# Performance work log

Measured on AMD Instinct MI355X. Metric: run time of the kernel, lower is better.

## Reference

```python
import jax, jax.numpy as jnp
import numpy as np

EPS = 1e-7  # keras.backend.epsilon()
ROUTING_ITERS = 3

def squash(v, axis=-1):
    s2 = jnp.sum(jnp.square(v), axis=axis, keepdims=True)
    scale = s2 / (1.0 + s2) / jnp.sqrt(s2 + EPS)
    return scale * v

def setup_inputs() -> dict:
    key = jax.random.key(0)
    k1, k2 = jax.random.split(key)
    B, N_IN, D_IN = 128, 648, 16
    N_OUT, D_OUT = 32, 32
    x = jax.random.normal(k1, (B, N_IN, D_IN), dtype=jnp.float32)
    # glorot-uniform-ish scale for W: shape (N_in, num_caps, cap_dim, d_in)
    limit = np.sqrt(6.0 / (D_IN + D_OUT)).astype(np.float32)
    W = jax.random.uniform(k2, (N_IN, N_OUT, D_OUT, D_IN), dtype=jnp.float32,
                           minval=-limit, maxval=limit)
    return {"x": x, "W": W}

def reference(x, W):
    # prediction vectors u_hat: [B, N_in, N_out, D_out]
    # (original tiles inputs then matmuls W @ u; einsum fuses this)
    u_hat = jnp.einsum('njdi,bni->bnjd', W, x)
    B, N_in, N_out, _ = u_hat.shape
    logits = jnp.zeros((B, N_in, N_out, 1), dtype=u_hat.dtype)
    v = None
    for i in range(ROUTING_ITERS):
        c = jax.nn.softmax(logits, axis=2)                      # [B,N_in,N_out,1]
        s = jnp.sum(c * u_hat, axis=1, keepdims=True)           # [B,1,N_out,D_out]
        v = squash(s, axis=-1)                                  # [B,1,N_out,D_out]
        if i < ROUTING_ITERS - 1:
            agreement = jnp.sum(u_hat * v, axis=-1, keepdims=True)
            logits = logits + agreement
    return jnp.squeeze(v, axis=1)                               # [B,N_out,D_out]
```

## Files before the change

### kernel.cpp

```cpp
#include <hip/hip_runtime.h>
#include <hip/hip_fp16.h>
#include <math.h>


#define N_IN 648
#define ELEMS 131072

#define WF16_OFF 1048576
#define PARTS_OFF 22282240

#define PX_OFF 131072
#define LG 139264
#define ARENA 147456

typedef __attribute__((ext_vector_type(8))) _Float16 f16x8;
typedef __attribute__((ext_vector_type(16))) float f32x16;

union F16U { uint4 u; f16x8 f; };
union HU { __half h; unsigned short us; };

__device__ __forceinline__ unsigned pkh(float a, float b) {
  HU x, y; x.h = __float2half(a); y.h = __float2half(b);
  return (unsigned)x.us | ((unsigned)y.us << 16);
}
__device__ __forceinline__ float h2f(unsigned short u) {
  HU x; x.us = u; return __half2float(x.h);
}

__device__ __forceinline__ void writeW(char* wbuf, int jS, int d, const float4* r) {
  uint4 h0, h1;
  h0.x = pkh(r[0].x, r[0].y); h0.y = pkh(r[0].z, r[0].w);
  h0.z = pkh(r[1].x, r[1].y); h0.w = pkh(r[1].z, r[1].w);
  h1.x = pkh(r[2].x, r[2].y); h1.y = pkh(r[2].z, r[2].w);
  h1.z = pkh(r[3].x, r[3].y); h1.w = pkh(r[3].z, r[3].w);
  *(uint4*)(wbuf + jS * 1024 + d * 16) = h0;
  *(uint4*)(wbuf + jS * 1024 + 512 + d * 16) = h1;
}
__device__ __forceinline__ void loadW(float4* r, const float* __restrict__ W,
                                      int n, int jS, int d) {
  const float4* rp = (const float4*)(W + (size_t)n * 16384 + jS * 512 + d * 16);
  r[0] = rp[0]; r[1] = rp[1]; r[2] = rp[2]; r[3] = rp[3];
}

__global__ __launch_bounds__(512) void cvt_w_f16(const float* __restrict__ W,
                                                 char* __restrict__ wf) {
  const int n = blockIdx.x;
  const int t = threadIdx.x;
  const int jS = t >> 4, m = t & 15;
  float4 rA[4], rB[4];
  loadW(rA, W, n, jS, m);
  loadW(rB, W, n, jS, m + 16);
  char* dst = wf + (size_t)n * 32768;
  writeW(dst, jS, m, rA);
  writeW(dst, jS, m + 16, rB);
}

__device__ __forceinline__ void stage_pair(char* nwf, char* nxb,
                                           const char* __restrict__ wf16,
                                           const float* __restrict__ x,
                                           int nbase, int cnt, int b0, int t) {
  const char* src = wf16 + (size_t)nbase * 32768;
  for (int r = 0; r < cnt * 4; ++r)
    *(uint4*)(nwf + r * 8192 + t * 16) = *(const uint4*)(src + r * 8192 + t * 16);
  if (t < 128) {
    const int s2 = t >> 6, u = t & 63;
    if (s2 < cnt) {
      const float4* xp = (const float4*)(
          x + ((size_t)(b0 + (u & 31)) * N_IN + nbase + s2) * 16 + (u >> 5) * 8);
      *(float4*)(nxb + s2 * 2048 + u * 16) = xp[0];
      *(float4*)(nxb + s2 * 2048 + 1024 + u * 16) = xp[1];
    }
  }
}

__device__ __forceinline__ void store_parts(char* arena, __half* __restrict__ parts,
                                            const f32x16* acc, float scale,
                                            int nchunk, int b0, int t) {
  const int w = t >> 6, l = t & 63;
  const int b32 = l & 31, half = l >> 5;
  __syncthreads();
#pragma unroll
  for (int q = 0; q < 4; ++q) {
    const int j = w * 4 + q;
#pragma unroll
    for (int g = 0; g < 4; ++g) {
      float4 v4;
      v4.x = acc[q][g * 4 + 0] * scale;
      v4.y = acc[q][g * 4 + 1] * scale;
      v4.z = acc[q][g * 4 + 2] * scale;
      v4.w = acc[q][g * 4 + 3] * scale;
      *(float4*)(arena + (b32 * 1036 + j * 32 + g * 8 + 4 * half) * 4) = v4;
    }
  }
  __syncthreads();
  char* pb = (char*)(parts + (size_t)nchunk * ELEMS + (size_t)b0 * 1024);
  const int rb = t >> 4, c16 = t & 15;
#pragma unroll
  for (int q = 0; q < 8; ++q) {
    const int g8 = c16 + q * 16;
    const float4 a = *(const float4*)(arena + (rb * 1036 + g8 * 8) * 4);
    const float4 b = *(const float4*)(arena + (rb * 1036 + g8 * 8 + 4) * 4);
    *(uint4*)(pb + rb * 2048 + g8 * 16) =
        uint4{pkh(a.x, a.y), pkh(a.z, a.w), pkh(b.x, b.y), pkh(b.z, b.w)};
  }
}

__device__ __forceinline__ void decode_bid(int bid, int NC, int& nchunk, int& btile) {
  if ((NC & 7) == 0) {
    const int r = bid & 7;
    btile = (bid >> 3) & 3;
    nchunk = (bid >> 5) * 8 + r;
  } else {
    nchunk = bid >> 2;
    btile = bid & 3;
  }
}

__global__ __launch_bounds__(512, 1) void caps_pass0_mfma(
    const float* __restrict__ x, const char* __restrict__ wf16,
    __half* __restrict__ parts, int NC)
{
  __shared__ __align__(16) char arena[ARENA];
  const int t = threadIdx.x;
  const int w = t >> 6, l = t & 63;
  int nchunk, btile;
  decode_bid(blockIdx.x, NC, nchunk, btile);
  const int n0 = (N_IN * nchunk) / NC;
  const int n1 = (N_IN * (nchunk + 1)) / NC;
  const int b0 = btile * 32;

  f32x16 acc[4];
#pragma unroll
  for (int q = 0; q < 4; ++q) acc[q] = (f32x16)(0.0f);

  stage_pair(arena, arena + PX_OFF, wf16, x, n0, (n1 - n0 >= 2) ? 2 : 1, b0, t);

  int cur = 0;
  for (int base = n0; base < n1; base += 2) {
    const int cnt = (n1 - base >= 2) ? 2 : 1;
    __syncthreads();
    const char* wf = arena + cur * 65536;
    const char* xb = arena + PX_OFF + cur * 4096;

    for (int s = 0; s < cnt; ++s) {
      const float4 xw0 = *(const float4*)(xb + s * 2048 + l * 16);
      const float4 xw1 = *(const float4*)(xb + s * 2048 + 1024 + l * 16);
      F16U bf;
      bf.u = uint4{pkh(xw0.x, xw0.y), pkh(xw0.z, xw0.w),
                   pkh(xw1.x, xw1.y), pkh(xw1.z, xw1.w)};
#pragma unroll
      for (int q = 0; q < 4; ++q) {
        const int j = w * 4 + q;
        const f16x8 af = *(const f16x8*)(wf + s * 32768 + j * 1024 + l * 16);
        acc[q] = __builtin_amdgcn_mfma_f32_32x32x16_f16(af, bf.f, acc[q], 0, 0, 0);
      }
    }

    if (base + 2 < n1) {
      const int ncnt = (n1 - (base + 2) >= 2) ? 2 : 1;
      stage_pair(arena + (cur ^ 1) * 65536, arena + PX_OFF + (cur ^ 1) * 4096,
                 wf16, x, base + 2, ncnt, b0, t);
    }
    cur ^= 1;
  }
  store_parts(arena, parts, acc, 0.03125f, nchunk, b0, t);
}

__global__ __launch_bounds__(512, 1) void caps_phase_mfma(
    const float* __restrict__ x, const char* __restrict__ wf16,
    const float* __restrict__ v,
    __half* __restrict__ parts, int NC)
{
  __shared__ __align__(16) char arena[ARENA];
  const int t = threadIdx.x;
  const int w = t >> 6, l = t & 63;
  const int b32 = l & 31, half = l >> 5;
  int nchunk, btile;
  decode_bid(blockIdx.x, NC, nchunk, btile);
  const int n0 = (N_IN * nchunk) / NC;
  const int n1 = (N_IN * (nchunk + 1)) / NC;
  const int b0 = btile * 32;

  unsigned vw[4][8];
  {
    const int bv = b0 + b32;
#pragma unroll
    for (int q = 0; q < 4; ++q) {
      const int j = w * 4 + q;
#pragma unroll
      for (int g = 0; g < 4; ++g) {
        const float4 g4 = *(const float4*)(v + (size_t)bv * 1024 + j * 32 + g * 8 + 4 * half);
        vw[q][2 * g]     = pkh(g4.x, g4.y);
        vw[q][2 * g + 1] = pkh(g4.z, g4.w);
      }
    }
  }

  stage_pair(arena, arena + PX_OFF, wf16, x, n0, (n1 - n0 >= 2) ? 2 : 1, b0, t);

  f32x16 acc[4];
#pragma unroll
  for (int q = 0; q < 4; ++q) acc[q] = (f32x16)(0.0f);

  int cur = 0;
  for (int base = n0; base < n1; base += 2) {
    const int cnt = (n1 - base >= 2) ? 2 : 1;
    __syncthreads();
    const char* wf = arena + cur * 65536;
    const char* xb = arena + PX_OFF + cur * 4096;

    for (int s = 0; s < cnt; ++s) {
      const float4 xw0 = *(const float4*)(xb + s * 2048 + l * 16);
      const float4 xw1 = *(const float4*)(xb + s * 2048 + 1024 + l * 16);
      F16U bf;
      bf.u = uint4{pkh(xw0.x, xw0.y), pkh(xw0.z, xw0.w),
                   pkh(xw1.x, xw1.y), pkh(xw1.z, xw1.w)};
#pragma unroll
      for (int q = 0; q < 4; ++q) {
        const int j = w * 4 + q;
        const f16x8 af = *(const f16x8*)(wf + s * 32768 + j * 1024 + l * 16);
        f32x16 ut = (f32x16)(0.0f);
        ut = __builtin_amdgcn_mfma_f32_32x32x16_f16(af, bf.f, ut, 0, 0, 0);
        float a = 0.f;
#pragma unroll
        for (int k = 0; k < 16; ++k) {
          const unsigned short us = (k & 1) ? (unsigned short)(vw[q][k >> 1] >> 16)
                                            : (unsigned short)(vw[q][k >> 1] & 0xFFFF);
          a = fmaf(ut[k], h2f(us), a);
        }
        a += __shfl_xor(a, 32);
        if (l < 32)
          *(float*)(arena + LG + s * 4096 + (j * 32 + ((b32 ^ j) & 31)) * 4) = a;
      }
    }
    __syncthreads();

    {
      const int jj = t & 31;
      for (int s = 0; s < cnt; ++s) {
#pragma unroll
        for (int r = 0; r < 2; ++r) {
          const int b = r * 16 + (t >> 5);
          float* slot = (float*)(arena + LG + s * 4096 + (jj * 32 + ((b ^ jj) & 31)) * 4);
          float lgv = *slot;
          float mx = lgv;
#pragma unroll
          for (int off = 16; off >= 1; off >>= 1) mx = fmaxf(mx, __shfl_xor(mx, off));
          const float e = __expf(lgv - mx);
          float Z = e;
#pragma unroll
          for (int off = 16; off >= 1; off >>= 1) Z += __shfl_xor(Z, off);
          *slot = e / Z;
        }
      }
    }

    if (base + 2 < n1) {
      const int ncnt = (n1 - (base + 2) >= 2) ? 2 : 1;
      stage_pair(arena + (cur ^ 1) * 65536, arena + PX_OFF + (cur ^ 1) * 4096,
                 wf16, x, base + 2, ncnt, b0, t);
    }
    __syncthreads();

    for (int s = 0; s < cnt; ++s) {
      const float4 xw0 = *(const float4*)(xb + s * 2048 + l * 16);
      const float4 xw1 = *(const float4*)(xb + s * 2048 + 1024 + l * 16);
#pragma unroll
      for (int q = 0; q < 4; ++q) {
        const int j = w * 4 + q;
        const float cj = *(const float*)(arena + LG + s * 4096 + (j * 32 + ((b32 ^ j) & 31)) * 4);
        F16U yf;
        yf.u = uint4{pkh(cj * xw0.x, cj * xw0.y), pkh(cj * xw0.z, cj * xw0.w),
                     pkh(cj * xw1.x, cj * xw1.y), pkh(cj * xw1.z, cj * xw1.w)};
        const f16x8 af = *(const f16x8*)(wf + s * 32768 + j * 1024 + l * 16);
        acc[q] = __builtin_amdgcn_mfma_f32_32x32x16_f16(af, yf.f, acc[q], 0, 0, 0);
      }
    }
    cur ^= 1;
  }
  store_parts(arena, parts, acc, 1.0f, nchunk, b0, t);
}

__global__ void reduce_squash(const unsigned short* __restrict__ parts, int NC,
                              float* __restrict__ out,
                              const float* __restrict__ addprev) {
  const int e = blockIdx.x * 256 + threadIdx.x;
  float s = 0.f;
  for (int c = 0; c < NC; ++c) s += h2f(parts[(size_t)c * ELEMS + e]);
  float s2 = s * s;
#pragma unroll
  for (int off = 16; off >= 1; off >>= 1) s2 += __shfl_xor(s2, off);
  const float scale = (s2 / (1.0f + s2)) * rsqrtf(s2 + 1e-7f);
  const float val = s * scale;
  out[e] = addprev ? (addprev[e] + val) : val;
}

extern "C" void kernel_launch(void* const* d_in, const int* in_sizes, int n_in,
                              void* d_out, int out_size, void* d_ws, size_t ws_size,
                              hipStream_t stream) {
  const float* x = (const float*)d_in[0];
  const float* W = (const float*)d_in[1];
  float* out = (float*)d_out;

  float* v0 = (float*)d_ws;
  float* vsum = v0 + ELEMS;
  char* wf16 = (char*)d_ws + WF16_OFF;
  __half* parts = (__half*)((char*)d_ws + PARTS_OFF);

  size_t rem = ws_size > (size_t)PARTS_OFF ? ws_size - PARTS_OFF : 0;
  int NC = (int)(rem / (ELEMS * 2));
  NC = NC < 1 ? 1 : (NC > 64 ? 64 : NC);

  const dim3 blk(512);

  cvt_w_f16<<<dim3(N_IN), blk, 0, stream>>>(W, wf16);

  caps_pass0_mfma<<<dim3(NC * 4), blk, 0, stream>>>(x, wf16, parts, NC);
  reduce_squash<<<512, 256, 0, stream>>>((const unsigned short*)parts, NC, v0, nullptr);

  caps_phase_mfma<<<dim3(NC * 4), blk, 0, stream>>>(x, wf16, v0, parts, NC);
  reduce_squash<<<512, 256, 0, stream>>>((const unsigned short*)parts, NC, vsum, v0);

  caps_phase_mfma<<<dim3(NC * 4), blk, 0, stream>>>(x, wf16, vsum, parts, NC);
  reduce_squash<<<512, 256, 0, stream>>>((const unsigned short*)parts, NC, out, nullptr);
}
```

Before: 152.1 us.

## Run routing phase kernel with 1024 threads, one input capsule per stage

The routing-phase kernel now launches 1024 threads (16 waves), each owning two output capsules instead of four. Staging moves from pairs of input capsules to single-capsule double buffering, which halves LDS use so the kernel can hold more waves. The partial-sum store is rewritten inline with a two-round LDS transpose. The aim is more latency hiding and less per-wave serial work, paid for with extra barriers per input capsule and lower register headroom per thread.

```diff
diff --git a/kernel.cpp b/kernel.cpp
--- a/kernel.cpp
+++ b/kernel.cpp
@@ -9,9 +9,12 @@
 #define WF16_OFF 1048576
 #define PARTS_OFF 22282240
 
-#define PX_OFF 131072
-#define LG 139264
-#define ARENA 147456
+#define P0X_OFF 131072
+#define ARENA_P0 147456
+
+#define XF_OFF 65536
+#define LG 69632
+#define ARENA_PH 73728
 
 typedef __attribute__((ext_vector_type(8))) _Float16 f16x8;
 typedef __attribute__((ext_vector_type(16))) float f32x16;
@@ -120,7 +123,7 @@
     const float* __restrict__ x, const char* __restrict__ wf16,
     __half* __restrict__ parts, int NC)
 {
-  __shared__ __align__(16) char arena[ARENA];
+  __shared__ __align__(16) char arena[ARENA_P0];
   const int t = threadIdx.x;
   const int w = t >> 6, l = t & 63;
   int nchunk, btile;
@@ -133,14 +136,14 @@
 #pragma unroll
   for (int q = 0; q < 4; ++q) acc[q] = (f32x16)(0.0f);
 
-  stage_pair(arena, arena + PX_OFF, wf16, x, n0, (n1 - n0 >= 2) ? 2 : 1, b0, t);
+  stage_pair(arena, arena + P0X_OFF, wf16, x, n0, (n1 - n0 >= 2) ? 2 : 1, b0, t);
 
   int cur = 0;
   for (int base = n0; base < n1; base += 2) {
     const int cnt = (n1 - base >= 2) ? 2 : 1;
     __syncthreads();
     const char* wf = arena + cur * 65536;
-    const char* xb = arena + PX_OFF + cur * 4096;
+    const char* xb = arena + P0X_OFF + cur * 4096;
 
     for (int s = 0; s < cnt; ++s) {
       const float4 xw0 = *(const float4*)(xb + s * 2048 + l * 16);
@@ -158,7 +161,7 @@
 
     if (base + 2 < n1) {
       const int ncnt = (n1 - (base + 2) >= 2) ? 2 : 1;
-      stage_pair(arena + (cur ^ 1) * 65536, arena + PX_OFF + (cur ^ 1) * 4096,
+      stage_pair(arena + (cur ^ 1) * 65536, arena + P0X_OFF + (cur ^ 1) * 4096,
                  wf16, x, base + 2, ncnt, b0, t);
     }
     cur ^= 1;
@@ -166,12 +169,12 @@
   store_parts(arena, parts, acc, 0.03125f, nchunk, b0, t);
 }
 
-__global__ __launch_bounds__(512, 1) void caps_phase_mfma(
+__global__ __launch_bounds__(1024, 1) void caps_phase_mfma(
     const float* __restrict__ x, const char* __restrict__ wf16,
     const float* __restrict__ v,
     __half* __restrict__ parts, int NC)
 {
-  __shared__ __align__(16) char arena[ARENA];
+  __shared__ __align__(16) char arena[ARENA_PH];
   const int t = threadIdx.x;
   const int w = t >> 6, l = t & 63;
   const int b32 = l & 31, half = l >> 5;
@@ -181,12 +184,12 @@
   const int n1 = (N_IN * (nchunk + 1)) / NC;
   const int b0 = btile * 32;
 
-  unsigned vw[4][8];
+  unsigned vw[2][8];
   {
     const int bv = b0 + b32;
 #pragma unroll
-    for (int q = 0; q < 4; ++q) {
-      const int j = w * 4 + q;
+    for (int q = 0; q < 2; ++q) {
+      const int j = w * 2 + q;
 #pragma unroll
       for (int g = 0; g < 4; ++g) {
         const float4 g4 = *(const float4*)(v + (size_t)bv * 1024 + j * 32 + g * 8 + 4 * half);
@@ -196,89 +199,125 @@
     }
   }
 
-  stage_pair(arena, arena + PX_OFF, wf16, x, n0, (n1 - n0 >= 2) ? 2 : 1, b0, t);
-
-  f32x16 acc[4];
-#pragma unroll
-  for (int q = 0; q < 4; ++q) acc[q] = (f32x16)(0.0f);
+  {
+    const char* src = wf16 + (size_t)n0 * 32768;
+    *(uint4*)(arena + t * 16) = *(const uint4*)(src + t * 16);
+    *(uint4*)(arena + 16384 + t * 16) = *(const uint4*)(src + 16384 + t * 16);
+    if (t < 64) {
+      const float4* xp = (const float4*)(x + ((size_t)(b0 + (t & 31)) * N_IN + n0) * 16 + (t >> 5) * 8);
+      *(float4*)(arena + XF_OFF + t * 16) = xp[0];
+      *(float4*)(arena + XF_OFF + 1024 + t * 16) = xp[1];
+    }
+  }
+
+  f32x16 acc[2];
+  acc[0] = (f32x16)(0.0f);
+  acc[1] = (f32x16)(0.0f);
 
   int cur = 0;
-  for (int base = n0; base < n1; base += 2) {
-    const int cnt = (n1 - base >= 2) ? 2 : 1;
-    __syncthreads();
-    const char* wf = arena + cur * 65536;
-    const char* xb = arena + PX_OFF + cur * 4096;
-
-    for (int s = 0; s < cnt; ++s) {
-      const float4 xw0 = *(const float4*)(xb + s * 2048 + l * 16);
-      const float4 xw1 = *(const float4*)(xb + s * 2048 + 1024 + l * 16);
-      F16U bf;
-      bf.u = uint4{pkh(xw0.x, xw0.y), pkh(xw0.z, xw0.w),
-                   pkh(xw1.x, xw1.y), pkh(xw1.z, xw1.w)};
-#pragma unroll
-      for (int q = 0; q < 4; ++q) {
-        const int j = w * 4 + q;
-        const f16x8 af = *(const f16x8*)(wf + s * 32768 + j * 1024 + l * 16);
-        f32x16 ut = (f32x16)(0.0f);
-        ut = __builtin_amdgcn_mfma_f32_32x32x16_f16(af, bf.f, ut, 0, 0, 0);
-        float a = 0.f;
-#pragma unroll
-        for (int k = 0; k < 16; ++k) {
-          const unsigned short us = (k & 1) ? (unsigned short)(vw[q][k >> 1] >> 16)
-                                            : (unsigned short)(vw[q][k >> 1] & 0xFFFF);
-          a = fmaf(ut[k], h2f(us), a);
+  for (int n = n0; n < n1; ++n) {
+    __syncthreads();
+    const char* wf = arena + cur * 32768;
+    const char* xb = arena + XF_OFF + cur * 2048;
+    char* nwf = arena + (cur ^ 1) * 32768;
+    char* nxb = arena + XF_OFF + (cur ^ 1) * 2048;
+    const bool more = (n + 1 < n1);
+
+    const float4 xw0 = *(const float4*)(xb + l * 16);
+    const float4 xw1 = *(const float4*)(xb + 1024 + l * 16);
+    F16U bf;
+    bf.u = uint4{pkh(xw0.x, xw0.y), pkh(xw0.z, xw0.w),
+                 pkh(xw1.x, xw1.y), pkh(xw1.z, xw1.w)};
+
+#pragma unroll
+    for (int q = 0; q < 2; ++q) {
+      const int j = w * 2 + q;
+      const f16x8 af = *(const f16x8*)(wf + j * 1024 + l * 16);
+      f32x16 ut = (f32x16)(0.0f);
+      ut = __builtin_amdgcn_mfma_f32_32x32x16_f16(af, bf.f, ut, 0, 0, 0);
+      float a = 0.f;
+#pragma unroll
+      for (int k = 0; k < 16; ++k) {
+        const unsigned short us = (k & 1) ? (unsigned short)(vw[q][k >> 1] >> 16)
+                                          : (unsigned short)(vw[q][k >> 1] & 0xFFFF);
+        a = fmaf(ut[k], h2f(us), a);
+      }
+      a += __shfl_xor(a, 32);
+      if (l < 32)
+        *(float*)(arena + LG + (j * 32 + ((b32 ^ j) & 31)) * 4) = a;
+    }
+    __syncthreads();
+
+    {
+      const int jj = t & 31, b = (w << 1) | (l >> 5);
+      float* slot = (float*)(arena + LG + (jj * 32 + ((b ^ jj) & 31)) * 4);
+      float lgv = *slot;
+      float mx = lgv;
+#pragma unroll
+      for (int off = 16; off >= 1; off >>= 1) mx = fmaxf(mx, __shfl_xor(mx, off));
+      const float e = __expf(lgv - mx);
+      float Z = e;
+#pragma unroll
+      for (int off = 16; off >= 1; off >>= 1) Z += __shfl_xor(Z, off);
+      *slot = e / Z;
+    }
+
+    if (more) {
+      const char* src = wf16 + (size_t)(n + 1) * 32768;
+      *(uint4*)(nwf + t * 16) = *(const uint4*)(src + t * 16);
+      *(uint4*)(nwf + 16384 + t * 16) = *(const uint4*)(src + 16384 + t * 16);
+      if (t < 64) {
+        const float4* xp = (const float4*)(x + ((size_t)(b0 + (t & 31)) * N_IN + n + 1) * 16 + (t >> 5) * 8);
+        *(float4*)(nxb + t * 16) = xp[0];
+        *(float4*)(nxb + 1024 + t * 16) = xp[1];
+      }
+    }
+    __syncthreads();
+
+#pragma unroll
+    for (int q = 0; q < 2; ++q) {
+      const int j = w * 2 + q;
+      const float cj = *(const float*)(arena + LG + (j * 32 + ((b32 ^ j) & 31)) * 4);
+      F16U yf;
+      yf.u = uint4{pkh(cj * xw0.x, cj * xw0.y), pkh(cj * xw0.z, cj * xw0.w),
+                   pkh(cj * xw1.x, cj * xw1.y), pkh(cj * xw1.z, cj * xw1.w)};
+      const f16x8 af = *(const f16x8*)(wf + j * 1024 + l * 16);
+      acc[q] = __builtin_amdgcn_mfma_f32_32x32x16_f16(af, yf.f, acc[q], 0, 0, 0);
+    }
+    cur ^= 1;
+  }
+
+#pragma unroll
+  for (int r = 0; r < 2; ++r) {
+    __syncthreads();
+    if ((b32 >> 4) == r) {
+      const int b16 = b32 & 15;
+#pragma unroll
+      for (int q = 0; q < 2; ++q) {
+        const int j = w * 2 + q;
+#pragma unroll
+        for (int g = 0; g < 4; ++g) {
+          float4 v4;
+          v4.x = acc[q][g * 4 + 0];
+          v4.y = acc[q][g * 4 + 1];
+          v4.z = acc[q][g * 4 + 2];
+          v4.w = acc[q][g * 4 + 3];
+          *(float4*)(arena + (b16 * 1036 + j * 32 + g * 8 + 4 * half) * 4) = v4;
         }
-        a += __shfl_xor(a, 32);
-        if (l < 32)
-          *(float*)(arena + LG + s * 4096 + (j * 32 + ((b32 ^ j) & 31)) * 4) = a;
-      }
-    }
-    __syncthreads();
-
-    {
-      const int jj = t & 31;
-      for (int s = 0; s < cnt; ++s) {
-#pragma unroll
-        for (int r = 0; r < 2; ++r) {
-          const int b = r * 16 + (t >> 5);
-          float* slot = (float*)(arena + LG + s * 4096 + (jj * 32 + ((b ^ jj) & 31)) * 4);
-          float lgv = *slot;
-          float mx = lgv;
-#pragma unroll
-          for (int off = 16; off >= 1; off >>= 1) mx = fmaxf(mx, __shfl_xor(mx, off));
-          const float e = __expf(lgv - mx);
-          float Z = e;
-#pragma unroll
-          for (int off = 16; off >= 1; off >>= 1) Z += __shfl_xor(Z, off);
-          *slot = e / Z;
-        }
-      }
-    }
-
-    if (base + 2 < n1) {
-      const int ncnt = (n1 - (base + 2) >= 2) ? 2 : 1;
-      stage_pair(arena + (cur ^ 1) * 65536, arena + PX_OFF + (cur ^ 1) * 4096,
-                 wf16, x, base + 2, ncnt, b0, t);
-    }
-    __syncthreads();
-
-    for (int s = 0; s < cnt; ++s) {
-      const float4 xw0 = *(const float4*)(xb + s * 2048 + l * 16);
-      const float4 xw1 = *(const float4*)(xb + s * 2048 + 1024 + l * 16);
-#pragma unroll
-      for (int q = 0; q < 4; ++q) {
-        const int j = w * 4 + q;
-        const float cj = *(const float*)(arena + LG + s * 4096 + (j * 32 + ((b32 ^ j) & 31)) * 4);
-        F16U yf;
-        yf.u = uint4{pkh(cj * xw0.x, cj * xw0.y), pkh(cj * xw0.z, cj * xw0.w),
-                     pkh(cj * xw1.x, cj * xw1.y), pkh(cj * xw1.z, cj * xw1.w)};
-        const f16x8 af = *(const f16x8*)(wf + s * 32768 + j * 1024 + l * 16);
-        acc[q] = __builtin_amdgcn_mfma_f32_32x32x16_f16(af, yf.f, acc[q], 0, 0, 0);
-      }
-    }
-    cur ^= 1;
-  }
-  store_parts(arena, parts, acc, 1.0f, nchunk, b0, t);
+      }
+    }
+    __syncthreads();
+    char* pb = (char*)(parts + (size_t)nchunk * ELEMS + (size_t)(b0 + r * 16) * 1024);
+    const int rb = t >> 6, c64 = t & 63;
+#pragma unroll
+    for (int q2 = 0; q2 < 2; ++q2) {
+      const int g8 = c64 + q2 * 64;
+      const float4 a = *(const float4*)(arena + (rb * 1036 + g8 * 8) * 4);
+      const float4 b = *(const float4*)(arena + (rb * 1036 + g8 * 8 + 4) * 4);
+      *(uint4*)(pb + rb * 2048 + g8 * 16) =
+          uint4{pkh(a.x, a.y), pkh(a.z, a.w), pkh(b.x, b.y), pkh(b.z, b.w)};
+    }
+  }
 }
 
 __global__ void reduce_squash(const unsigned short* __restrict__ parts, int NC,
@@ -312,15 +351,16 @@
   NC = NC < 1 ? 1 : (NC > 64 ? 64 : NC);
 
   const dim3 blk(512);
+  const dim3 blkP(1024);
 
   cvt_w_f16<<<dim3(N_IN), blk, 0, stream>>>(W, wf16);
 
   caps_pass0_mfma<<<dim3(NC * 4), blk, 0, stream>>>(x, wf16, parts, NC);
   reduce_squash<<<512, 256, 0, stream>>>((const unsigned short*)parts, NC, v0, nullptr);
 
-  caps_phase_mfma<<<dim3(NC * 4), blk, 0, stream>>>(x, wf16, v0, parts, NC);
+  caps_phase_mfma<<<dim3(NC * 4), blkP, 0, stream>>>(x, wf16, v0, parts, NC);
   reduce_squash<<<512, 256, 0, stream>>>((const unsigned short*)parts, NC, vsum, v0);
 
-  caps_phase_mfma<<<dim3(NC * 4), blk, 0, stream>>>(x, wf16, vsum, parts, NC);
+  caps_phase_mfma<<<dim3(NC * 4), blkP, 0, stream>>>(x, wf16, vsum, parts, NC);
   reduce_squash<<<512, 256, 0, stream>>>((const unsigned short*)parts, NC, out, nullptr);
 }
```

Result: faster. 141.5 us (-7.0%).
